# Performance work log

Hardware: AMD Instinct MI355X
Metric: run time of the kernel (lower is better)

Reference implementation:

```python
import jax, jax.numpy as jnp
import numpy as np

POOL_LEN = 256
EPS = 1e-5
WEIGHT_BITS = 2


def adaptive_avg_pool1d(x, out_len):
    """Faithful torch AdaptiveAvgPool1d: window i = [floor(i*L/out), ceil((i+1)*L/out)).
    Implemented via cumsum + static gathers (jit-friendly, vectorized)."""
    L = x.shape[-1]
    i = np.arange(out_len)
    starts = (i * L) // out_len
    ends = -((-(i + 1) * L) // out_len)  # integer ceil
    csum = jnp.cumsum(x, axis=-1)
    csum = jnp.concatenate([jnp.zeros(x.shape[:-1] + (1,), x.dtype), csum], axis=-1)
    counts = jnp.asarray(ends - starts, x.dtype)
    return (csum[..., ends] - csum[..., starts]) / counts


def quantize_weight(w, bits=WEIGHT_BITS):
    """2-bit symmetric uniform quantization, per-output-channel scale, STE."""
    qp = 2 ** (bits - 1) - 1          # +1
    qn = -(2 ** (bits - 1))           # -2
    scale = jnp.maximum(jnp.max(jnp.abs(w), axis=1, keepdims=True) / qp, 1e-8)
    w_q = jnp.clip(jnp.round(w / scale), qn, qp) * scale
    return w + jax.lax.stop_gradient(w_q - w)  # straight-through estimator


def setup_inputs() -> dict:
    key = jax.random.key(0)
    k1, k2, k3, kw = jax.random.split(key, 4)
    B = 64
    return {
        "stage1": jax.random.normal(k1, (B, 256, 5000), jnp.float32),
        "stage2": jax.random.normal(k2, (B, 128, 2500), jnp.float32),
        "stage3": jax.random.normal(k3, (B, 64, 625), jnp.float32),
        "alpha": jnp.ones((3,), jnp.float32) / 3.0,
        "weight": jax.random.normal(kw, (128, 448), jnp.float32) * 0.05,
        "bias": jnp.zeros((128,), jnp.float32),
        "gamma": jnp.ones((128,), jnp.float32),
        "beta": jnp.zeros((128,), jnp.float32),
    }


def reference(stage1, stage2, stage3, alpha, weight, bias, gamma, beta):
    w = jax.nn.softmax(alpha)
    s1 = adaptive_avg_pool1d(stage1, POOL_LEN) * w[0]
    s2 = adaptive_avg_pool1d(stage2, POOL_LEN) * w[1]
    s3 = adaptive_avg_pool1d(stage3, POOL_LEN) * w[2]
    fused = jnp.concatenate([s1, s2, s3], axis=1)  # (B, 448, 256)
    wq = quantize_weight(weight)
    y = jnp.einsum('oc,bcl->bol', wq, fused) + bias[None, :, None]  # (B, 128, 256)
    # BatchNorm1d (training mode: batch stats over N and L)
    mean = jnp.mean(y, axis=(0, 2))
    var = jnp.var(y, axis=(0, 2))
    yn = (y - mean[None, :, None]) * jax.lax.rsqrt(var + EPS)[None, :, None]
    yn = yn * gamma[None, :, None] + beta[None, :, None]
    act = jax.nn.elu(yn)
    return jnp.mean(act, axis=-1)  # (B, 128)
```

## Files before the change

kernel.cpp:

```cpp
#include <hip/hip_runtime.h>
#include <hip/hip_bf16.h>

#define EPSV 1e-5f

typedef __attribute__((ext_vector_type(8))) short short8v;
typedef __attribute__((ext_vector_type(4))) short short4v;
typedef __attribute__((ext_vector_type(4))) float float4v;

__device__ inline unsigned short f2bf(float x) {
  __hip_bfloat16 h = __float2bfloat16(x);
  return *reinterpret_cast<unsigned short*>(&h);
}
__device__ inline float bf2f(unsigned short b) {
  unsigned u = ((unsigned)b) << 16;
  float f;
  __builtin_memcpy(&f, &u, 4);
  return f;
}

__device__ __forceinline__ void bar_lds() {
  asm volatile("s_waitcnt lgkmcnt(0)\n\ts_barrier" ::: "memory");
}

template <int L, int MAXW, int ROWS, int CH, int CHOFF>
__device__ __forceinline__ void pool_rows_vec(
    const float* __restrict__ srcBase, int row0, float wst,
    unsigned short* __restrict__ fusedb, float* __restrict__ row, int t) {
  constexpr int L4 = L / 4;
  constexpr int NLD = (L4 + 255) / 256;
  float4v buf[NLD];
  {
    const float4v* rp = (const float4v*)(srcBase + (size_t)row0 * L);
    #pragma unroll
    for (int i = 0; i < NLD; ++i) {
      int idx = t + 256 * i;
      if (NLD * 256 == L4 || idx < L4) buf[i] = __builtin_nontemporal_load(rp + idx);
    }
  }
  if (t < MAXW) row[L + t] = 0.f;
  #pragma unroll 1
  for (int r = 0; r < ROWS; ++r) {
    #pragma unroll
    for (int i = 0; i < NLD; ++i) {
      int idx = t + 256 * i;
      if (NLD * 256 == L4 || idx < L4) *(float4v*)&row[idx * 4] = buf[i];
    }
    bar_lds();
    if (r + 1 < ROWS) {
      const float4v* rpn = (const float4v*)(srcBase + (size_t)(row0 + r + 1) * L);
      #pragma unroll
      for (int i = 0; i < NLD; ++i) {
        int idx = t + 256 * i;
        if (NLD * 256 == L4 || idx < L4) buf[i] = __builtin_nontemporal_load(rpn + idx);
      }
    }
    int start = (t * L) >> 8;
    int end = ((t + 1) * L + 255) >> 8;
    int width = end - start;
    float s = 0.f;
    #pragma unroll
    for (int i = 0; i < MAXW; ++i) {
      float v = row[start + i];
      s += (i < width) ? v : 0.f;
    }
    int rr = row0 + r;
    int b = rr / CH, c = rr % CH;
    fusedb[((size_t)b * 448 + CHOFF + c) * 256 + t] = f2bf(s / (float)width * wst);
    bar_lds();
  }
}

template <int L, int MAXW, int ROWS, int CH, int CHOFF>
__device__ __forceinline__ void pool_rows_scalar(
    const float* __restrict__ srcBase, int row0, float wst,
    unsigned short* __restrict__ fusedb, float* __restrict__ row, int t) {
  constexpr int NLD = (L + 255) / 256;
  float buf[NLD];
  {
    const float* rp = srcBase + (size_t)row0 * L;
    #pragma unroll
    for (int i = 0; i < NLD; ++i) {
      int idx = t + 256 * i;
      if (idx < L) buf[i] = __builtin_nontemporal_load(rp + idx);
    }
  }
  if (t < MAXW) row[L + t] = 0.f;
  #pragma unroll 1
  for (int r = 0; r < ROWS; ++r) {
    #pragma unroll
    for (int i = 0; i < NLD; ++i) {
      int idx = t + 256 * i;
      if (idx < L) row[idx] = buf[i];
    }
    bar_lds();
    if (r + 1 < ROWS) {
      const float* rpn = srcBase + (size_t)(row0 + r + 1) * L;
      #pragma unroll
      for (int i = 0; i < NLD; ++i) {
        int idx = t + 256 * i;
        if (idx < L) buf[i] = __builtin_nontemporal_load(rpn + idx);
      }
    }
    int start = (t * L) >> 8;
    int end = ((t + 1) * L + 255) >> 8;
    int width = end - start;
    float s = 0.f;
    #pragma unroll
    for (int i = 0; i < MAXW; ++i) {
      float v = row[start + i];
      s += (i < width) ? v : 0.f;
    }
    int rr = row0 + r;
    int b = rr / CH, c = rr % CH;
    fusedb[((size_t)b * 448 + CHOFF + c) * 256 + t] = f2bf(s / (float)width * wst);
    bar_lds();
  }
}

__global__ __launch_bounds__(256) void pool_quant_kernel(
    const float* __restrict__ s1, const float* __restrict__ s2,
    const float* __restrict__ s3, const float* __restrict__ alpha,
    const float* __restrict__ w, unsigned short* __restrict__ fusedb,
    unsigned short* __restrict__ qbf, float* __restrict__ scales) {
  __shared__ float row[5024];
  int bid = blockIdx.x;
  int t = threadIdx.x;

  if (bid >= 5376) {
    int o = bid - 5376;
    const float* wr = w + o * 448;
    float m = 0.f;
    for (int c = t; c < 448; c += 256) m = fmaxf(m, fabsf(wr[c]));
    float* sm = row;
    for (int off = 32; off; off >>= 1) m = fmaxf(m, __shfl_down(m, off, 64));
    if ((t & 63) == 0) sm[t >> 6] = m;
    __syncthreads();
    m = fmaxf(fmaxf(sm[0], sm[1]), fmaxf(sm[2], sm[3]));
    float scale = fmaxf(m, 1e-8f);
    for (int c = t; c < 448; c += 256) {
      float q = rintf(wr[c] / scale);
      q = fminf(fmaxf(q, -2.f), 1.f);
      qbf[o * 448 + c] = f2bf(q);
    }
    if (t == 0) scales[o] = scale;
    return;
  }

  float a0 = alpha[0], a1 = alpha[1], a2 = alpha[2];
  float mx = fmaxf(a0, fmaxf(a1, a2));
  float e0 = expf(a0 - mx), e1 = expf(a1 - mx), e2 = expf(a2 - mx);
  float esum = e0 + e1 + e2;

  if (bid < 4096) {
    pool_rows_vec<5000, 21, 4, 256, 0>(s1, bid * 4, e0 / esum, fusedb, row, t);
  } else if (bid < 5120) {
    pool_rows_vec<2500, 11, 8, 128, 256>(s2, (bid - 4096) * 8, e1 / esum, fusedb, row, t);
  } else {
    pool_rows_scalar<625, 4, 16, 64, 384>(s3, (bid - 5120) * 16, e2 / esum, fusedb, row, t);
  }
}

__global__ __launch_bounds__(256) void mfma_gemm_kernel(
    const unsigned short* __restrict__ qbf, const float* __restrict__ scales,
    const unsigned short* __restrict__ fusedb, const float* __restrict__ bias,
    unsigned short* __restrict__ ybf, float* __restrict__ Psum,
    float* __restrict__ Pssq) {
  __shared__ __align__(16) unsigned short Asm[64][40];
  __shared__ __align__(16) unsigned Bsm32[16][66];
  int b = blockIdx.z;
  int o0 = blockIdx.y * 64;
  int l0 = blockIdx.x * 64;
  int tid = threadIdx.x;
  int wave = tid >> 6, lane = tid & 63;
  int wm = wave >> 1, wn = wave & 1;
  int lrow = lane & 15, lg = lane >> 4;
  const unsigned short* Fp = fusedb + (size_t)b * 448 * 256;
  float4v acc[2][2];
  #pragma unroll
  for (int i = 0; i < 2; ++i)
    #pragma unroll
    for (int j = 0; j < 2; ++j) acc[i][j] = (float4v){0.f, 0.f, 0.f, 0.f};
  for (int c0 = 0; c0 < 448; c0 += 32) {
    { int r = tid >> 2, k0 = (tid & 3) * 8;
      *(short8v*)&Asm[r][k0] = *(const short8v*)(qbf + (size_t)(o0 + r) * 448 + c0 + k0); }
    {
      int kp = tid >> 4, n0 = (tid & 15) * 4;
      const unsigned short* g0 = Fp + (size_t)(c0 + 2 * kp) * 256 + l0 + n0;
      short4v v0 = *(const short4v*)g0;
      short4v v1 = *(const short4v*)(g0 + 256);
      #pragma unroll
      for (int j = 0; j < 4; ++j)
        Bsm32[kp][n0 + j] =
            (((unsigned)(unsigned short)v1[j]) << 16) | (unsigned short)v0[j];
    }
    __syncthreads();
    short8v af[2];
    #pragma unroll
    for (int mf = 0; mf < 2; ++mf)
      af[mf] = *(const short8v*)&Asm[wm * 32 + mf * 16 + lrow][lg * 8];
    #pragma unroll
    for (int nf = 0; nf < 2; ++nf) {
      int n = wn * 32 + nf * 16 + lrow;
      int tmp[4];
      #pragma unroll
      for (int jj = 0; jj < 4; ++jj) tmp[jj] = (int)Bsm32[lg * 4 + jj][n];
      short8v bf;
      __builtin_memcpy(&bf, tmp, 16);
      #pragma unroll
      for (int mf = 0; mf < 2; ++mf)
        acc[mf][nf] = __builtin_amdgcn_mfma_f32_16x16x32_bf16(af[mf], bf, acc[mf][nf], 0, 0, 0);
    }
    __syncthreads();
  }
  float sv[2][4], qv[2][4];
  #pragma unroll
  for (int mf = 0; mf < 2; ++mf) {
    #pragma unroll
    for (int reg = 0; reg < 4; ++reg) {
      int r = o0 + wm * 32 + mf * 16 + lg * 4 + reg;
      float sc = scales[r], bv = bias[r];
      float s = 0.f, q = 0.f;
      #pragma unroll
      for (int nf = 0; nf < 2; ++nf) {
        int col = l0 + wn * 32 + nf * 16 + lrow;
        float val = acc[mf][nf][reg] * sc + bv;
        ybf[((size_t)b * 128 + r) * 256 + col] = f2bf(val);
        s += val; q += val * val;
      }
      sv[mf][reg] = s; qv[mf][reg] = q;
    }
  }
  #pragma unroll
  for (int mf = 0; mf < 2; ++mf)
    #pragma unroll
    for (int reg = 0; reg < 4; ++reg)
      #pragma unroll
      for (int m = 1; m < 16; m <<= 1) {
        sv[mf][reg] += __shfl_xor(sv[mf][reg], m, 64);
        qv[mf][reg] += __shfl_xor(qv[mf][reg], m, 64);
      }
  if (lrow == 0) {
    int slot = b * 8 + blockIdx.x * 2 + wn;
    #pragma unroll
    for (int mf = 0; mf < 2; ++mf)
      #pragma unroll
      for (int reg = 0; reg < 4; ++reg) {
        int r = o0 + wm * 32 + mf * 16 + lg * 4 + reg;
        Psum[r * 512 + slot] = sv[mf][reg];
        Pssq[r * 512 + slot] = qv[mf][reg];
      }
  }
}

__global__ __launch_bounds__(256) void final_kernel(
    const unsigned short* __restrict__ ybf, const float* __restrict__ Psum,
    const float* __restrict__ Pssq, const float* __restrict__ gamma,
    const float* __restrict__ beta, float* __restrict__ out) {
  int w = threadIdx.x >> 6;
  int lane = threadIdx.x & 63;
  int bo = blockIdx.x * 4 + w;
  int o = bo & 127;

  float s = 0.f, q = 0.f;
  const float* Pp = Psum + o * 512 + lane * 8;
  const float* Qp = Pssq + o * 512 + lane * 8;
  #pragma unroll
  for (int i = 0; i < 8; ++i) { s += Pp[i]; q += Qp[i]; }
  #pragma unroll
  for (int m = 1; m < 64; m <<= 1) {
    s += __shfl_xor(s, m, 64);
    q += __shfl_xor(q, m, 64);
  }
  float mean = s * (1.f / 16384.f);
  float var = q * (1.f / 16384.f) - mean * mean;
  float rs = rsqrtf(var + EPSV);
  float a = rs * gamma[o];
  float bb = beta[o] - mean * a;

  ushort4 v = *(const ushort4*)(ybf + (size_t)bo * 256 + lane * 4);
  float acc = 0.f;
  #pragma unroll
  for (int j = 0; j < 4; ++j) {
    float e = bf2f((&v.x)[j]);
    float yn = e * a + bb;
    acc += yn > 0.f ? yn : expm1f(yn);
  }
  for (int m = 32; m; m >>= 1) acc += __shfl_down(acc, m, 64);
  if (lane == 0) out[bo] = acc * (1.f / 256.f);
}

extern "C" void kernel_launch(void* const* d_in, const int* in_sizes, int n_in,
                              void* d_out, int out_size, void* d_ws, size_t ws_size,
                              hipStream_t stream) {
  const float* s1     = (const float*)d_in[0];
  const float* s2     = (const float*)d_in[1];
  const float* s3     = (const float*)d_in[2];
  const float* alpha  = (const float*)d_in[3];
  const float* weight = (const float*)d_in[4];
  const float* bias   = (const float*)d_in[5];
  const float* gamma  = (const float*)d_in[6];
  const float* beta   = (const float*)d_in[7];
  float* out = (float*)d_out;

  char* ws = (char*)d_ws;
  unsigned short* fusedb = (unsigned short*)ws;
  unsigned short* qbf    = (unsigned short*)(ws + 14680064);
  float* scales          = (float*)(ws + 14794752);
  unsigned short* ybf    = (unsigned short*)(ws + 14795264);
  float* Psum            = (float*)(ws + 18989568);
  float* Pssq            = (float*)(ws + 19251712);

  pool_quant_kernel<<<5504, 256, 0, stream>>>(s1, s2, s3, alpha, weight,
                                              fusedb, qbf, scales);
  dim3 g(4, 2, 64);
  mfma_gemm_kernel<<<g, 256, 0, stream>>>(qbf, scales, fusedb, bias, ybf,
                                          Psum, Pssq);
  final_kernel<<<2048, 256, 0, stream>>>(ybf, Psum, Pssq, gamma, beta, out);
}
```

Baseline: 101.0 us.

## Stream pooling rows into double-buffered LDS via global_load_lds DMA

Replaces the register-staged row loads in the stage1/stage2 pooling with direct global-to-LDS loads into two LDS buffers, prefetching row r+2 while row r is being reduced. Stage1 blocks now handle 8 rows instead of 4, so the grid shrinks and the block index ranges are remapped. The aim is to drop the register round trip and overlap memory traffic with the window reductions. In exchange it doubles LDS use per block, which may lower occupancy, and depends on hand-written vmcnt waits matching the number of loads each wave has in flight.

```diff
diff --git a/kernel.cpp b/kernel.cpp
--- a/kernel.cpp
+++ b/kernel.cpp
@@ -18,55 +18,73 @@
   return f;
 }
 
+__device__ __forceinline__ void bar_raw() {
+  asm volatile("s_barrier" ::: "memory");
+}
 __device__ __forceinline__ void bar_lds() {
   asm volatile("s_waitcnt lgkmcnt(0)\n\ts_barrier" ::: "memory");
 }
-
-template <int L, int MAXW, int ROWS, int CH, int CHOFF>
-__device__ __forceinline__ void pool_rows_vec(
+template <int N>
+__device__ __forceinline__ void wait_vmcnt() {
+  if constexpr (N == 0) asm volatile("s_waitcnt vmcnt(0)" ::: "memory");
+  else if constexpr (N == 3) asm volatile("s_waitcnt vmcnt(3)" ::: "memory");
+  else if constexpr (N == 5) asm volatile("s_waitcnt vmcnt(5)" ::: "memory");
+}
+
+__device__ __forceinline__ void gload_lds16(const float* g, float* l) {
+  __builtin_amdgcn_global_load_lds(
+      (const __attribute__((address_space(1))) void*)(unsigned long long)(uintptr_t)g,
+      (__attribute__((address_space(3))) void*)l, 16, 0, 0);
+}
+
+template <int NC, int CPW, int TAIL_LANES>
+__device__ __forceinline__ void issue_row(
+    const float* __restrict__ rowp, float* __restrict__ buf, int wv, int lane) {
+  #pragma unroll
+  for (int j = 0; j < CPW; ++j) {
+    int c = wv * CPW + j;
+    if (c > NC - 1) c = NC - 1;
+    const float* g = rowp + c * 256 + lane * 4;
+    float* l = buf + c * 256;
+    if (c == NC - 1) {
+      if (lane < TAIL_LANES) gload_lds16(g, l);
+    } else {
+      gload_lds16(g, l);
+    }
+  }
+}
+
+template <int L, int MAXW, int ROWS, int CH, int CHOFF, int NC, int CPW, int TAIL_LANES>
+__device__ __forceinline__ void pool_rows_dma(
     const float* __restrict__ srcBase, int row0, float wst,
-    unsigned short* __restrict__ fusedb, float* __restrict__ row, int t) {
-  constexpr int L4 = L / 4;
-  constexpr int NLD = (L4 + 255) / 256;
-  float4v buf[NLD];
-  {
-    const float4v* rp = (const float4v*)(srcBase + (size_t)row0 * L);
-    #pragma unroll
-    for (int i = 0; i < NLD; ++i) {
-      int idx = t + 256 * i;
-      if (NLD * 256 == L4 || idx < L4) buf[i] = __builtin_nontemporal_load(rp + idx);
-    }
-  }
-  if (t < MAXW) row[L + t] = 0.f;
-  #pragma unroll 1
+    unsigned short* __restrict__ fusedb, float* __restrict__ buf0,
+    float* __restrict__ buf1, int t) {
+  int wv = t >> 6, lane = t & 63;
+  issue_row<NC, CPW, TAIL_LANES>(srcBase + (size_t)row0 * L, buf0, wv, lane);
+  issue_row<NC, CPW, TAIL_LANES>(srcBase + (size_t)(row0 + 1) * L, buf1, wv, lane);
+  if (t < MAXW) { buf0[L + t] = 0.f; buf1[L + t] = 0.f; }
+  asm volatile("s_waitcnt lgkmcnt(0)" ::: "memory");
+  #pragma unroll
   for (int r = 0; r < ROWS; ++r) {
-    #pragma unroll
-    for (int i = 0; i < NLD; ++i) {
-      int idx = t + 256 * i;
-      if (NLD * 256 == L4 || idx < L4) *(float4v*)&row[idx * 4] = buf[i];
-    }
-    bar_lds();
-    if (r + 1 < ROWS) {
-      const float4v* rpn = (const float4v*)(srcBase + (size_t)(row0 + r + 1) * L);
-      #pragma unroll
-      for (int i = 0; i < NLD; ++i) {
-        int idx = t + 256 * i;
-        if (NLD * 256 == L4 || idx < L4) buf[i] = __builtin_nontemporal_load(rpn + idx);
-      }
-    }
+    float* cur = (r & 1) ? buf1 : buf0;
+    if (r < ROWS - 1) wait_vmcnt<CPW>();
+    else wait_vmcnt<0>();
+    bar_raw();
     int start = (t * L) >> 8;
     int end = ((t + 1) * L + 255) >> 8;
     int width = end - start;
     float s = 0.f;
     #pragma unroll
     for (int i = 0; i < MAXW; ++i) {
-      float v = row[start + i];
+      float v = cur[start + i];
       s += (i < width) ? v : 0.f;
     }
     int rr = row0 + r;
     int b = rr / CH, c = rr % CH;
     fusedb[((size_t)b * 448 + CHOFF + c) * 256 + t] = f2bf(s / (float)width * wst);
-    bar_lds();
+    bar_raw();
+    if (r + 2 < ROWS)
+      issue_row<NC, CPW, TAIL_LANES>(srcBase + (size_t)(row0 + r + 2) * L, cur, wv, lane);
   }
 }
 
@@ -122,16 +140,16 @@
     const float* __restrict__ s3, const float* __restrict__ alpha,
     const float* __restrict__ w, unsigned short* __restrict__ fusedb,
     unsigned short* __restrict__ qbf, float* __restrict__ scales) {
-  __shared__ float row[5024];
+  __shared__ float pool_lds[2][5024];
   int bid = blockIdx.x;
   int t = threadIdx.x;
 
-  if (bid >= 5376) {
-    int o = bid - 5376;
+  if (bid >= 3328) {
+    int o = bid - 3328;
     const float* wr = w + o * 448;
     float m = 0.f;
     for (int c = t; c < 448; c += 256) m = fmaxf(m, fabsf(wr[c]));
-    float* sm = row;
+    float* sm = pool_lds[0];
     for (int off = 32; off; off >>= 1) m = fmaxf(m, __shfl_down(m, off, 64));
     if ((t & 63) == 0) sm[t >> 6] = m;
     __syncthreads();
@@ -151,12 +169,15 @@
   float e0 = expf(a0 - mx), e1 = expf(a1 - mx), e2 = expf(a2 - mx);
   float esum = e0 + e1 + e2;
 
-  if (bid < 4096) {
-    pool_rows_vec<5000, 21, 4, 256, 0>(s1, bid * 4, e0 / esum, fusedb, row, t);
-  } else if (bid < 5120) {
-    pool_rows_vec<2500, 11, 8, 128, 256>(s2, (bid - 4096) * 8, e1 / esum, fusedb, row, t);
+  if (bid < 2048) {
+    pool_rows_dma<5000, 21, 8, 256, 0, 20, 5, 34>(
+        s1, bid * 8, e0 / esum, fusedb, pool_lds[0], pool_lds[1], t);
+  } else if (bid < 3072) {
+    pool_rows_dma<2500, 11, 8, 128, 256, 10, 3, 49>(
+        s2, (bid - 2048) * 8, e1 / esum, fusedb, pool_lds[0], pool_lds[1], t);
   } else {
-    pool_rows_scalar<625, 4, 16, 64, 384>(s3, (bid - 5120) * 16, e2 / esum, fusedb, row, t);
+    pool_rows_scalar<625, 4, 16, 64, 384>(
+        s3, (bid - 3072) * 16, e2 / esum, fusedb, pool_lds[0], t);
   }
 }
 
@@ -183,8 +204,7 @@
   for (int c0 = 0; c0 < 448; c0 += 32) {
     { int r = tid >> 2, k0 = (tid & 3) * 8;
       *(short8v*)&Asm[r][k0] = *(const short8v*)(qbf + (size_t)(o0 + r) * 448 + c0 + k0); }
-    {
-      int kp = tid >> 4, n0 = (tid & 15) * 4;
+    { int kp = tid >> 4, n0 = (tid & 15) * 4;
       const unsigned short* g0 = Fp + (size_t)(c0 + 2 * kp) * 256 + l0 + n0;
       short4v v0 = *(const short4v*)g0;
       short4v v1 = *(const short4v*)(g0 + 256);
@@ -310,7 +330,7 @@
   float* Psum            = (float*)(ws + 18989568);
   float* Pssq            = (float*)(ws + 19251712);
 
-  pool_quant_kernel<<<5504, 256, 0, stream>>>(s1, s2, s3, alpha, weight,
+  pool_quant_kernel<<<3456, 256, 0, stream>>>(s1, s2, s3, alpha, weight,
                                               fusedb, qbf, scales);
   dim3 g(4, 2, 64);
   mfma_gemm_kernel<<<g, 256, 0, stream>>>(qbf, scales, fusedb, bias, ybf,
```

Result: slower. 110.0 us (+8.8%).
